# Kernel tuning notes

Hardware: AMD Instinct MI355X
Metric: run time of the kernel (lower is better)

## Reference

```python
import jax, jax.numpy as jnp
import numpy as np

HEADS = 8
NEG = -1e9
EPS = 1e-9


def setup_inputs() -> dict:
    key = jax.random.key(0)
    ks = jax.random.split(key, 24)
    N, D, E = 2048, 512, 64
    s = 0.02
    inp = {
        "xyz": jax.random.normal(ks[0], (N, 3), jnp.float32),
        "str_feat": jax.random.normal(ks[1], (N, D), jnp.float32),
        "esm_feat": jax.random.normal(ks[2], (N, E), jnp.float32),
        "y_hat": jax.random.uniform(ks[3], (N, 1), jnp.float32),
        "distance_mask": jax.random.randint(ks[4], (N, N), 0, 2, jnp.int32),
        "t": jnp.ones((1,), jnp.float32),
        "band_width": jnp.ones((1,), jnp.float32),
        "max_iter": 5,
        # main projections (torch Linear layout: y = x @ W.T + b)
        "Wq": jax.random.normal(ks[5], (D, D), jnp.float32) * s,
        "bq": jnp.zeros((D,), jnp.float32),
        "Wk": jax.random.normal(ks[6], (D, D), jnp.float32) * s,
        "bk": jnp.zeros((D,), jnp.float32),
        "Wv": jax.random.normal(ks[7], (D, D), jnp.float32) * s,
        "bv": jnp.zeros((D,), jnp.float32),
        "Wo": jax.random.normal(ks[8], (D, D), jnp.float32) * s,
        "bo": jnp.zeros((D,), jnp.float32),
        # esm projections (computed in the original forward but unused downstream)
        "Weq": jax.random.normal(ks[9], (E, E), jnp.float32) * s,
        "beq": jnp.zeros((E,), jnp.float32),
        "Wek": jax.random.normal(ks[10], (E, E), jnp.float32) * s,
        "bek": jnp.zeros((E,), jnp.float32),
        "Wev": jax.random.normal(ks[11], (E, E), jnp.float32) * s,
        "bev": jnp.zeros((E,), jnp.float32),
        "Weo": jax.random.normal(ks[12], (E, E), jnp.float32) * s,
        "beo": jnp.zeros((E,), jnp.float32),
    }
    return inp


def reference(xyz, str_feat, esm_feat, y_hat, distance_mask, t, band_width, max_iter,
              Wq, bq, Wk, bk, Wv, bv, Wo, bo,
              Weq, beq, Wek, bek, Wev, bev, Weo, beo):
    N, D = str_feat.shape
    h = HEADS
    dh = D // h

    q = str_feat @ Wq.T + bq
    k = str_feat @ Wk.T + bk
    v = str_feat @ Wv.T + bv
    # esm projections: computed in the original forward but never used (dead code; DCE'd under jit)
    _esm_q = esm_feat @ Weq.T + beq
    _esm_k = esm_feat @ Wek.T + bek
    _esm_v = esm_feat @ Wev.T + bev

    # [h, N, dh]
    qh = q.reshape(N, h, dh).transpose(1, 0, 2)
    kh = k.reshape(N, h, dh).transpose(1, 0, 2)
    vh = v.reshape(N, h, dh).transpose(1, 0, 2)

    scores = jnp.einsum('hnd,hmd->hnm', qh, kh) / jnp.sqrt(jnp.asarray(dh, qh.dtype))
    mask = (distance_mask > 0)[None]              # [1, N, N]
    yw = y_hat[:, 0][None, :]                     # [1, N] per-target weight
    inv_two_bw2 = 1.0 / (2.0 * band_width[0] ** 2)
    temp = t[0]

    def step(carry, _):
        xyz_c, _x = carry
        # squared pairwise distances via the expanded form (avoids [N,N,3])
        sq = jnp.sum(xyz_c * xyz_c, axis=-1)
        d2 = sq[:, None] + sq[None, :] - 2.0 * (xyz_c @ xyz_c.T)
        kern = jnp.exp(-d2 * inv_two_bw2)          # [N, N] band-width kernel
        logits = scores / temp + jnp.log(kern * yw + EPS)[None]
        logits = jnp.where(mask, logits, NEG)
        attn = jax.nn.softmax(logits, axis=-1)     # [h, N, N]
        xyz_new = jnp.einsum('nm,md->nd', attn.mean(0), xyz_c)  # mean-shift step
        x_new = jnp.einsum('hnm,hmd->hnd', attn, vh)            # [h, N, dh]
        return (xyz_new, x_new), None

    (xyz_out, xh), _ = jax.lax.scan(step, (xyz, jnp.zeros_like(vh)), None, length=max_iter)
    x = xh.transpose(1, 0, 2).reshape(N, D)
    out = x @ Wo.T + bo
    return xyz_out, out
```

## Files before the change

kernel.cpp:

```cpp
#include <hip/hip_runtime.h>


typedef __attribute__((ext_vector_type(8))) short bf16x8;
typedef __attribute__((ext_vector_type(4))) float f32x4;

__device__ __forceinline__ unsigned short f2bf(float f) {
    unsigned int u = __float_as_uint(f);
    u += 0x7fff + ((u >> 16) & 1);
    return (unsigned short)(u >> 16);
}
__device__ __forceinline__ float bf2f(unsigned short u) {
    return __uint_as_float((unsigned int)u << 16);
}

union EU { bf16x8 v; unsigned short u[8]; };

__global__ __launch_bounds__(256)
void conv_all(const float* __restrict__ strf,
              const float* __restrict__ Wq, const float* __restrict__ Wk,
              const float* __restrict__ Wv, const float* __restrict__ Wo,
              const int* __restrict__ dmask,
              unsigned short* __restrict__ sA, unsigned short* __restrict__ sW,
              unsigned char* __restrict__ mby)
{
    const long base = (long)(blockIdx.x * 256 + threadIdx.x) * 8;
    if (base >= 2097152) {
        const long rel = base - 2097152;
        int4 a = *reinterpret_cast<const int4*>(dmask + rel);
        int4 b = *reinterpret_cast<const int4*>(dmask + rel + 4);
        unsigned long long p = 0;
        p |= (a.x > 0) ? 0x01ULL : 0;  p |= (a.y > 0) ? 0x0100ULL : 0;
        p |= (a.z > 0) ? 0x010000ULL : 0;  p |= (a.w > 0) ? 0x01000000ULL : 0;
        p |= (b.x > 0) ? 0x0100000000ULL : 0;  p |= (b.y > 0) ? 0x010000000000ULL : 0;
        p |= (b.z > 0) ? 0x01000000000000ULL : 0;  p |= (b.w > 0) ? 0x0100000000000000ULL : 0;
        *reinterpret_cast<unsigned long long*>(mby + rel) = p;
        return;
    }
    const float* src;
    unsigned short* dst;
    if (base < 1048576) {
        src = strf + base; dst = sA + base;
    } else {
        const long rel = base - 1048576;
        const int seg = (int)(rel >> 18);
        const long off = rel & 262143;
        const float* Ws[4] = {Wq, Wk, Wv, Wo};
        src = Ws[seg] + off;
        dst = sW + (long)seg * 262144 + off;
    }
    float4 a = *reinterpret_cast<const float4*>(src);
    float4 b = *reinterpret_cast<const float4*>(src + 4);
    EU o;
    o.u[0] = f2bf(a.x); o.u[1] = f2bf(a.y); o.u[2] = f2bf(a.z); o.u[3] = f2bf(a.w);
    o.u[4] = f2bf(b.x); o.u[5] = f2bf(b.y); o.u[6] = f2bf(b.z); o.u[7] = f2bf(b.w);
    *reinterpret_cast<bf16x8*>(dst) = o.v;
}

__global__ __launch_bounds__(256)
void qkv_mfma(const unsigned short* __restrict__ sA,
              const unsigned short* __restrict__ sW,
              const float* __restrict__ bq, const float* __restrict__ bk,
              const float* __restrict__ bv,
              unsigned short* __restrict__ qh, unsigned short* __restrict__ kh,
              unsigned short* __restrict__ vT)
{
    const int z  = blockIdx.z;
    const int bx = blockIdx.x;
    const int by = blockIdx.y;
    const int tid = threadIdx.x;
    const int wv = tid >> 6;
    const int lane = tid & 63;
    const int row  = lane & 15;
    const int koct = (lane >> 4) * 8;
    const int n0 = bx * 64;

    const unsigned short* Ap = sA + (long)(n0 + wv * 16 + row) * 512;
    const unsigned short* Bp = sW + (long)z * 262144 + (long)(by * 64 + row) * 512;

    f32x4 acc[4] = {};
#pragma unroll
    for (int k0 = 0; k0 < 512; k0 += 32) {
        bf16x8 a = *reinterpret_cast<const bf16x8*>(Ap + k0 + koct);
#pragma unroll
        for (int t = 0; t < 4; t++) {
            bf16x8 b = *reinterpret_cast<const bf16x8*>(Bp + (long)(t * 16) * 512 + k0 + koct);
            acc[t] = __builtin_amdgcn_mfma_f32_16x16x32_bf16(a, b, acc[t], 0, 0, 0);
        }
    }

    if (z == 2) {
        const int rbase = n0 + wv * 16 + (lane >> 4) * 4;
#pragma unroll
        for (int t = 0; t < 4; t++) {
            const int d = by * 64 + t * 16 + (lane & 15);
            const float bb = bv[d];
            ushort4 o;
            o.x = f2bf(acc[t][0] + bb); o.y = f2bf(acc[t][1] + bb);
            o.z = f2bf(acc[t][2] + bb); o.w = f2bf(acc[t][3] + bb);
            *reinterpret_cast<ushort4*>(vT + (long)d * 2048 + rbase) = o;
        }
        return;
    }

    __shared__ float ls[64][68];
    const int lrb = wv * 16 + (lane >> 4) * 4;
    const int lcb = lane & 15;
#pragma unroll
    for (int t = 0; t < 4; t++)
#pragma unroll
        for (int r = 0; r < 4; r++)
            ls[lrb + r][t * 16 + lcb] = acc[t][r];
    __syncthreads();

    const float* bias = (z == 0) ? bq : bk;
    unsigned short* dst = (z == 0) ? qh : kh;
    const int r2 = tid >> 2;
    const int c2 = (tid & 3) * 16;
    float sv[16];
#pragma unroll
    for (int j = 0; j < 4; j++) {
        float4 s = *reinterpret_cast<const float4*>(&ls[r2][c2 + j * 4]);
        float4 bb = *reinterpret_cast<const float4*>(bias + by * 64 + c2 + j * 4);
        sv[j*4+0] = s.x + bb.x; sv[j*4+1] = s.y + bb.y;
        sv[j*4+2] = s.z + bb.z; sv[j*4+3] = s.w + bb.w;
    }
    EU o0, o1;
#pragma unroll
    for (int j = 0; j < 8; j++) { o0.u[j] = f2bf(sv[j]); o1.u[j] = f2bf(sv[8 + j]); }
    unsigned short* dp = dst + (long)(n0 + r2) * 512 + by * 64 + c2;
    *reinterpret_cast<bf16x8*>(dp)     = o0.v;
    *reinterpret_cast<bf16x8*>(dp + 8) = o1.v;
}

__global__ __launch_bounds__(256)
void scores_rows(const unsigned short* __restrict__ qh,
                 const unsigned short* __restrict__ kh,
                 const unsigned char* __restrict__ mby,
                 const float* __restrict__ tptr,
                 unsigned short* __restrict__ Ebf)
{
    const int h  = blockIdx.y;
    const int n0 = blockIdx.x * 16;
    const int tid = threadIdx.x;
    const int wv = tid >> 6;
    const int lane = tid & 63;
    const float scale = 1.0f / (8.0f * tptr[0]);

    __shared__ unsigned short lsb[4][16][260];

    const int arow = lane & 15;
    const int koct = (lane >> 4) * 8;
    const unsigned short* Aq = qh + (long)(n0 + arow) * 512 + h * 64;
    const bf16x8 aq0 = *reinterpret_cast<const bf16x8*>(Aq + koct);
    const bf16x8 aq1 = *reinterpret_cast<const bf16x8*>(Aq + 32 + koct);

    const int lr = (lane >> 4) * 4;
    const int lc = lane & 15;
    const int rlo = lane >> 5;
    const int cch = lane & 31;

#pragma unroll
    for (int half = 0; half < 2; half++) {
        const int mbase = wv * 512 + half * 256;
#pragma unroll
        for (int mt = 0; mt < 16; mt++) {
            const unsigned short* Bk = kh + (long)(mbase + mt * 16 + arow) * 512 + h * 64;
            bf16x8 b0 = *reinterpret_cast<const bf16x8*>(Bk + koct);
            bf16x8 b1 = *reinterpret_cast<const bf16x8*>(Bk + 32 + koct);
            f32x4 c = {};
            c = __builtin_amdgcn_mfma_f32_16x16x32_bf16(aq0, b0, c, 0, 0, 0);
            c = __builtin_amdgcn_mfma_f32_16x16x32_bf16(aq1, b1, c, 0, 0, 0);
#pragma unroll
            for (int r = 0; r < 4; r++)
                lsb[wv][lr + r][mt * 16 + lc] = f2bf(__expf(c[r] * scale));
        }
#pragma unroll
        for (int rp = 0; rp < 8; rp++) {
            const int row = rp * 2 + rlo;
            const int gn = n0 + row;
            const int m = mbase + cch * 8;
            EU e;
            e.v = *reinterpret_cast<const bf16x8*>(&lsb[wv][row][cch * 8]);
            unsigned long long mk =
                *reinterpret_cast<const unsigned long long*>(mby + (long)gn * 2048 + m);
            EU o;
#pragma unroll
            for (int j = 0; j < 8; j++)
                o.u[j] = ((mk >> (8 * j)) & 0xff) ? e.u[j] : (unsigned short)0;
            *reinterpret_cast<bf16x8*>(Ebf + ((long)h * 2048 + gn) * 2048 + m) = o.v;
        }
    }
}

__global__ __launch_bounds__(256)
void ms_iter(const unsigned short* __restrict__ Ebf,
             const float* __restrict__ xyz_src,
             float* __restrict__ xyz_dst,
             const float* __restrict__ y_hat,
             const float* __restrict__ bwp,
             unsigned short* __restrict__ gbf,
             float* __restrict__ invzb,
             int wlast)
{
    const int n = blockIdx.x;
    const int tid = threadIdx.x;
    const int lane = tid & 63;
    const int wave = tid >> 6;
    const int m0 = tid * 8;

    __shared__ float red[64];

    EU E[8];
#pragma unroll
    for (int h = 0; h < 8; h++)
        E[h].v = *reinterpret_cast<const bf16x8*>(Ebf + (long)h * 4194304 + (long)n * 2048 + m0);

    const float bw = bwp[0];
    const float c2k = 1.0f / (2.0f * bw * bw);

    const float xn = xyz_src[n * 3 + 0];
    const float yn = xyz_src[n * 3 + 1];
    const float zn = xyz_src[n * 3 + 2];
    const float sqn = xn * xn + yn * yn + zn * zn;

    float mx[8], my[8], mz[8];
    {
        const float4* xp = reinterpret_cast<const float4*>(xyz_src + (long)m0 * 3);
        float4 a = xp[0], b = xp[1], c = xp[2], d = xp[3], e = xp[4], f = xp[5];
        mx[0]=a.x; my[0]=a.y; mz[0]=a.z;  mx[1]=a.w; my[1]=b.x; mz[1]=b.y;
        mx[2]=b.z; my[2]=b.w; mz[2]=c.x;  mx[3]=c.y; my[3]=c.z; mz[3]=c.w;
        mx[4]=d.x; my[4]=d.y; mz[4]=d.z;  mx[5]=d.w; my[5]=e.x; mz[5]=e.y;
        mx[6]=e.z; my[6]=e.w; mz[6]=f.x;  mx[7]=f.y; my[7]=f.z; mz[7]=f.w;
    }
    float4 yh0 = *reinterpret_cast<const float4*>(y_hat + m0);
    float4 yh1 = *reinterpret_cast<const float4*>(y_hat + m0 + 4);
    float yh[8] = {yh0.x, yh0.y, yh0.z, yh0.w, yh1.x, yh1.y, yh1.z, yh1.w};

    float g[8];
#pragma unroll
    for (int j = 0; j < 8; j++) {
        const float d2 = sqn + (mx[j]*mx[j] + my[j]*my[j] + mz[j]*mz[j])
                       - 2.0f * (xn*mx[j] + yn*my[j] + zn*mz[j]);
        g[j] = __expf(-d2 * c2k) * yh[j] + 1e-9f;
    }

    float z[8];
#pragma unroll
    for (int h = 0; h < 8; h++) {
        float zz = 0.f;
#pragma unroll
        for (int j = 0; j < 8; j++) zz += bf2f(E[h].u[j]) * g[j];
        z[h] = zz;
    }

#pragma unroll
    for (int h = 0; h < 8; h++) {
        float v = z[h];
#pragma unroll
        for (int off = 32; off > 0; off >>= 1) v += __shfl_down(v, off, 64);
        if (lane == 0) red[wave * 8 + h] = v;
    }
    __syncthreads();
    if (tid < 8) {
        const float s = red[tid] + red[8 + tid] + red[16 + tid] + red[24 + tid];
        const float iz = 1.0f / s;
        red[32 + tid] = iz;
        if (wlast) invzb[tid * 2048 + n] = iz;
    }
    __syncthreads();
    float invz[8];
#pragma unroll
    for (int h = 0; h < 8; h++) invz[h] = red[32 + h];
    __syncthreads();

    float ax = 0.f, ay = 0.f, az = 0.f;
#pragma unroll
    for (int j = 0; j < 8; j++) {
        float w = 0.f;
#pragma unroll
        for (int h = 0; h < 8; h++) w += bf2f(E[h].u[j]) * invz[h];
        w *= 0.125f * g[j];
        ax += w * mx[j]; ay += w * my[j]; az += w * mz[j];
    }
    if (wlast) {
        EU og;
#pragma unroll
        for (int j = 0; j < 8; j++) og.u[j] = f2bf(g[j]);
        *reinterpret_cast<bf16x8*>(gbf + (long)n * 2048 + m0) = og.v;
    }

    float v3[3] = {ax, ay, az};
#pragma unroll
    for (int c = 0; c < 3; c++) {
        float v = v3[c];
#pragma unroll
        for (int off = 32; off > 0; off >>= 1) v += __shfl_down(v, off, 64);
        if (lane == 0) red[c * 4 + wave] = v;
    }
    __syncthreads();
    if (tid < 3) {
        xyz_dst[n * 3 + tid] = red[tid * 4 + 0] + red[tid * 4 + 1] +
                               red[tid * 4 + 2] + red[tid * 4 + 3];
    }
}

__global__ __launch_bounds__(256)
void av_mfma(const unsigned short* __restrict__ Ebf,
             const unsigned short* __restrict__ gbf,
             const unsigned short* __restrict__ vT,
             float* __restrict__ P)
{
    const int h  = blockIdx.z;
    const int s  = blockIdx.y;
    const int bx = blockIdx.x;
    const int wv = threadIdx.x >> 6;
    const int lane = threadIdx.x & 63;
    const int n0 = bx * 64 + wv * 16;
    const int kc = s * 512;

    const int mrow = lane & 15;
    const int koct = (lane >> 4) * 8;

    const unsigned short* Ab = Ebf + ((long)h * 2048 + n0 + mrow) * 2048;
    const unsigned short* Gb = gbf + (long)(n0 + mrow) * 2048;
    const unsigned short* Bb = vT + ((long)h * 64 + mrow) * 2048;

    f32x4 acc[4] = {};
    for (int k0 = kc; k0 < kc + 512; k0 += 32) {
        EU e, gg, a;
        e.v  = *reinterpret_cast<const bf16x8*>(Ab + k0 + koct);
        gg.v = *reinterpret_cast<const bf16x8*>(Gb + k0 + koct);
#pragma unroll
        for (int j = 0; j < 8; j++)
            a.u[j] = f2bf(bf2f(e.u[j]) * bf2f(gg.u[j]));
#pragma unroll
        for (int t = 0; t < 4; t++) {
            bf16x8 b = *reinterpret_cast<const bf16x8*>(Bb + (long)(t * 16) * 2048 + k0 + koct);
            acc[t] = __builtin_amdgcn_mfma_f32_16x16x32_bf16(a.v, b, acc[t], 0, 0, 0);
        }
    }

    float* Pp = P + (long)s * 1048576;
    const int rbase = n0 + (lane >> 4) * 4;
    const int dcol = lane & 15;
#pragma unroll
    for (int t = 0; t < 4; t++)
#pragma unroll
        for (int r = 0; r < 4; r++)
            Pp[(long)(rbase + r) * 512 + h * 64 + t * 16 + dcol] = acc[t][r];
}

__global__ __launch_bounds__(256)
void av_red(const float* __restrict__ P, const float* __restrict__ invzb,
            unsigned short* __restrict__ xc)
{
    const long idx = (long)(blockIdx.x * 256 + threadIdx.x) * 8;
    const int n = (int)(idx >> 9);
    const int d0 = (int)(idx & 511);
    const float iz = invzb[(d0 >> 6) * 2048 + n];
    float s[8] = {};
#pragma unroll
    for (int p = 0; p < 4; p++) {
        const float* pp = P + (long)p * 1048576 + idx;
        float4 a = *reinterpret_cast<const float4*>(pp);
        float4 b = *reinterpret_cast<const float4*>(pp + 4);
        s[0] += a.x; s[1] += a.y; s[2] += a.z; s[3] += a.w;
        s[4] += b.x; s[5] += b.y; s[6] += b.z; s[7] += b.w;
    }
    EU o;
#pragma unroll
    for (int j = 0; j < 8; j++) o.u[j] = f2bf(s[j] * iz);
    *reinterpret_cast<bf16x8*>(xc + idx) = o.v;
}

__global__ __launch_bounds__(256)
void out_mfma(const unsigned short* __restrict__ xc,
              const unsigned short* __restrict__ sW,
              const float* __restrict__ bo,
              float* __restrict__ out)
{
    const int bx = blockIdx.x;
    const int by = blockIdx.y;
    const int wv = threadIdx.x >> 6;
    const int lane = threadIdx.x & 63;
    const int row  = lane & 15;
    const int koct = (lane >> 4) * 8;
    const int n0 = bx * 64;

    const unsigned short* Ap = xc + (long)(n0 + wv * 16 + row) * 512;
    const unsigned short* Bp = sW + 3L * 262144 + (long)(by * 64 + row) * 512;

    f32x4 acc[4] = {};
#pragma unroll
    for (int k0 = 0; k0 < 512; k0 += 32) {
        bf16x8 a = *reinterpret_cast<const bf16x8*>(Ap + k0 + koct);
#pragma unroll
        for (int t = 0; t < 4; t++) {
            bf16x8 b = *reinterpret_cast<const bf16x8*>(Bp + (long)(t * 16) * 512 + k0 + koct);
            acc[t] = __builtin_amdgcn_mfma_f32_16x16x32_bf16(a, b, acc[t], 0, 0, 0);
        }
    }

    const int rbase = n0 + wv * 16 + (lane >> 4) * 4;
    const int dcol = lane & 15;
#pragma unroll
    for (int t = 0; t < 4; t++) {
        const int col = by * 64 + t * 16 + dcol;
        const float bb = bo[col];
#pragma unroll
        for (int r = 0; r < 4; r++)
            out[(long)(rbase + r) * 512 + col] = acc[t][r] + bb;
    }
}

extern "C" void kernel_launch(void* const* d_in, const int* in_sizes, int n_in,
                              void* d_out, int out_size, void* d_ws, size_t ws_size,
                              hipStream_t stream)
{
    (void)in_sizes; (void)n_in; (void)out_size; (void)ws_size;

    const float* xyz   = (const float*)d_in[0];
    const float* strf  = (const float*)d_in[1];
    const float* yhat  = (const float*)d_in[3];
    const int*   dmask = (const int*)d_in[4];
    const float* tptr  = (const float*)d_in[5];
    const float* bwptr = (const float*)d_in[6];
    const float* Wq = (const float*)d_in[8];
    const float* bq = (const float*)d_in[9];
    const float* Wk = (const float*)d_in[10];
    const float* bk = (const float*)d_in[11];
    const float* Wv = (const float*)d_in[12];
    const float* bv = (const float*)d_in[13];
    const float* Wo = (const float*)d_in[14];
    const float* bo = (const float*)d_in[15];
    float* outp = (float*)d_out;

    char* wsb = (char*)d_ws;
    float* Ppart         = (float*)(wsb);
    unsigned short* xc   = (unsigned short*)(wsb + (16L << 20));
    unsigned short* sA   = (unsigned short*)(wsb + (18L << 20));
    unsigned short* sW   = (unsigned short*)(wsb + (20L << 20));
    unsigned short* qh   = (unsigned short*)(wsb + (22L << 20));
    unsigned short* kh   = (unsigned short*)(wsb + (24L << 20));
    unsigned short* vT   = (unsigned short*)(wsb + (26L << 20));
    float* xyzA          = (float*)(wsb + (28L << 20));
    float* xyzB          = xyzA + 8192;
    unsigned char* mby   = (unsigned char*)(wsb + (30L << 20));
    unsigned short* Ebf  = (unsigned short*)(wsb + (34L << 20));
    unsigned short* gbf  = (unsigned short*)(wsb + (98L << 20));
    float* invzb         = (float*)(wsb + (106L << 20));

    dim3 blk(256, 1, 1);

    conv_all<<<dim3(3072), blk, 0, stream>>>(strf, Wq, Wk, Wv, Wo, dmask, sA, sW, mby);
    qkv_mfma<<<dim3(32, 8, 3), blk, 0, stream>>>(sA, sW, bq, bk, bv, qh, kh, vT);

    scores_rows<<<dim3(128, 8), blk, 0, stream>>>(qh, kh, mby, tptr, Ebf);

    const float* src = xyz;
    float* dsts[5] = {xyzA, xyzB, xyzA, xyzB, outp};
    for (int it = 0; it < 5; it++) {
        ms_iter<<<dim3(2048), blk, 0, stream>>>(Ebf, src, dsts[it], yhat, bwptr,
                                                gbf, invzb, it == 4 ? 1 : 0);
        src = dsts[it];
    }

    av_mfma<<<dim3(32, 4, 8), blk, 0, stream>>>(Ebf, gbf, vT, Ppart);
    av_red<<<dim3(512), blk, 0, stream>>>(Ppart, invzb, xc);
    out_mfma<<<dim3(32, 8), blk, 0, stream>>>(xc, sW, bo, outp + 6144);
}
```

Measured before the change: 325.3 us.

## Pack four rows per ms_iter block, double split-K in av_mfma with prefetch

```diff
diff --git a/kernel.cpp b/kernel.cpp
--- a/kernel.cpp
+++ b/kernel.cpp
@@ -192,7 +192,7 @@
     }
 }
 
-__global__ __launch_bounds__(256)
+__global__ __launch_bounds__(1024)
 void ms_iter(const unsigned short* __restrict__ Ebf,
              const float* __restrict__ xyz_src,
              float* __restrict__ xyz_dst,
@@ -202,46 +202,47 @@
              float* __restrict__ invzb,
              int wlast)
 {
-    const int n = blockIdx.x;
     const int tid = threadIdx.x;
+    const int rg  = tid >> 8;
+    const int t   = tid & 255;
+    const int n   = blockIdx.x * 4 + rg;
     const int lane = tid & 63;
-    const int wave = tid >> 6;
-    const int m0 = tid * 8;
-
-    __shared__ float red[64];
+    const int wv4 = (t >> 6) & 3;
+    const int m0 = t * 8;
+
+    __shared__ float red[4][52];
 
     EU E[8];
+    const unsigned short* Ep = Ebf + (long)n * 2048 + m0;
 #pragma unroll
     for (int h = 0; h < 8; h++)
-        E[h].v = *reinterpret_cast<const bf16x8*>(Ebf + (long)h * 4194304 + (long)n * 2048 + m0);
+        E[h].v = *reinterpret_cast<const bf16x8*>(Ep + (long)h * 4194304);
 
     const float bw = bwp[0];
     const float c2k = 1.0f / (2.0f * bw * bw);
-
     const float xn = xyz_src[n * 3 + 0];
     const float yn = xyz_src[n * 3 + 1];
     const float zn = xyz_src[n * 3 + 2];
     const float sqn = xn * xn + yn * yn + zn * zn;
 
-    float mx[8], my[8], mz[8];
+    float g[8];
     {
         const float4* xp = reinterpret_cast<const float4*>(xyz_src + (long)m0 * 3);
         float4 a = xp[0], b = xp[1], c = xp[2], d = xp[3], e = xp[4], f = xp[5];
+        float mx[8], my[8], mz[8];
         mx[0]=a.x; my[0]=a.y; mz[0]=a.z;  mx[1]=a.w; my[1]=b.x; mz[1]=b.y;
         mx[2]=b.z; my[2]=b.w; mz[2]=c.x;  mx[3]=c.y; my[3]=c.z; mz[3]=c.w;
         mx[4]=d.x; my[4]=d.y; mz[4]=d.z;  mx[5]=d.w; my[5]=e.x; mz[5]=e.y;
         mx[6]=e.z; my[6]=e.w; mz[6]=f.x;  mx[7]=f.y; my[7]=f.z; mz[7]=f.w;
-    }
-    float4 yh0 = *reinterpret_cast<const float4*>(y_hat + m0);
-    float4 yh1 = *reinterpret_cast<const float4*>(y_hat + m0 + 4);
-    float yh[8] = {yh0.x, yh0.y, yh0.z, yh0.w, yh1.x, yh1.y, yh1.z, yh1.w};
-
-    float g[8];
-#pragma unroll
-    for (int j = 0; j < 8; j++) {
-        const float d2 = sqn + (mx[j]*mx[j] + my[j]*my[j] + mz[j]*mz[j])
-                       - 2.0f * (xn*mx[j] + yn*my[j] + zn*mz[j]);
-        g[j] = __expf(-d2 * c2k) * yh[j] + 1e-9f;
+        float4 yh0 = *reinterpret_cast<const float4*>(y_hat + m0);
+        float4 yh1 = *reinterpret_cast<const float4*>(y_hat + m0 + 4);
+        float yh[8] = {yh0.x, yh0.y, yh0.z, yh0.w, yh1.x, yh1.y, yh1.z, yh1.w};
+#pragma unroll
+        for (int j = 0; j < 8; j++) {
+            const float d2 = sqn + (mx[j]*mx[j] + my[j]*my[j] + mz[j]*mz[j])
+                           - 2.0f * (xn*mx[j] + yn*my[j] + zn*mz[j]);
+            g[j] = __expf(-d2 * c2k) * yh[j] + 1e-9f;
+        }
     }
 
     float z[8];
@@ -258,29 +259,37 @@
         float v = z[h];
 #pragma unroll
         for (int off = 32; off > 0; off >>= 1) v += __shfl_down(v, off, 64);
-        if (lane == 0) red[wave * 8 + h] = v;
+        if (lane == 0) red[rg][wv4 * 8 + h] = v;
     }
     __syncthreads();
-    if (tid < 8) {
-        const float s = red[tid] + red[8 + tid] + red[16 + tid] + red[24 + tid];
+    if (t < 8) {
+        const float s = red[rg][t] + red[rg][8 + t] + red[rg][16 + t] + red[rg][24 + t];
         const float iz = 1.0f / s;
-        red[32 + tid] = iz;
-        if (wlast) invzb[tid * 2048 + n] = iz;
+        red[rg][32 + t] = iz;
+        if (wlast) invzb[t * 2048 + n] = iz;
     }
     __syncthreads();
     float invz[8];
 #pragma unroll
-    for (int h = 0; h < 8; h++) invz[h] = red[32 + h];
-    __syncthreads();
+    for (int h = 0; h < 8; h++) invz[h] = red[rg][32 + h];
 
     float ax = 0.f, ay = 0.f, az = 0.f;
-#pragma unroll
-    for (int j = 0; j < 8; j++) {
-        float w = 0.f;
-#pragma unroll
-        for (int h = 0; h < 8; h++) w += bf2f(E[h].u[j]) * invz[h];
-        w *= 0.125f * g[j];
-        ax += w * mx[j]; ay += w * my[j]; az += w * mz[j];
+    {
+        const float4* xp = reinterpret_cast<const float4*>(xyz_src + (long)m0 * 3);
+        float4 a = xp[0], b = xp[1], c = xp[2], d = xp[3], e = xp[4], f = xp[5];
+        float mx[8], my[8], mz[8];
+        mx[0]=a.x; my[0]=a.y; mz[0]=a.z;  mx[1]=a.w; my[1]=b.x; mz[1]=b.y;
+        mx[2]=b.z; my[2]=b.w; mz[2]=c.x;  mx[3]=c.y; my[3]=c.z; mz[3]=c.w;
+        mx[4]=d.x; my[4]=d.y; mz[4]=d.z;  mx[5]=d.w; my[5]=e.x; mz[5]=e.y;
+        mx[6]=e.z; my[6]=e.w; mz[6]=f.x;  mx[7]=f.y; my[7]=f.z; mz[7]=f.w;
+#pragma unroll
+        for (int j = 0; j < 8; j++) {
+            float w = 0.f;
+#pragma unroll
+            for (int h = 0; h < 8; h++) w += bf2f(E[h].u[j]) * invz[h];
+            w *= 0.125f * g[j];
+            ax += w * mx[j]; ay += w * my[j]; az += w * mz[j];
+        }
     }
     if (wlast) {
         EU og;
@@ -295,12 +304,12 @@
         float v = v3[c];
 #pragma unroll
         for (int off = 32; off > 0; off >>= 1) v += __shfl_down(v, off, 64);
-        if (lane == 0) red[c * 4 + wave] = v;
+        if (lane == 0) red[rg][40 + c * 4 + wv4] = v;
     }
     __syncthreads();
-    if (tid < 3) {
-        xyz_dst[n * 3 + tid] = red[tid * 4 + 0] + red[tid * 4 + 1] +
-                               red[tid * 4 + 2] + red[tid * 4 + 3];
+    if (t < 3) {
+        xyz_dst[n * 3 + t] = red[rg][40 + t * 4 + 0] + red[rg][40 + t * 4 + 1] +
+                             red[rg][40 + t * 4 + 2] + red[rg][40 + t * 4 + 3];
     }
 }
 
@@ -316,28 +325,36 @@
     const int wv = threadIdx.x >> 6;
     const int lane = threadIdx.x & 63;
     const int n0 = bx * 64 + wv * 16;
-    const int kc = s * 512;
+    const int kc = s * 256;
 
     const int mrow = lane & 15;
     const int koct = (lane >> 4) * 8;
 
-    const unsigned short* Ab = Ebf + ((long)h * 2048 + n0 + mrow) * 2048;
-    const unsigned short* Gb = gbf + (long)(n0 + mrow) * 2048;
-    const unsigned short* Bb = vT + ((long)h * 64 + mrow) * 2048;
+    const unsigned short* Ab = Ebf + ((long)h * 2048 + n0 + mrow) * 2048 + kc + koct;
+    const unsigned short* Gb = gbf + (long)(n0 + mrow) * 2048 + kc + koct;
+    const unsigned short* Bb = vT + ((long)h * 64 + mrow) * 2048 + kc + koct;
 
     f32x4 acc[4] = {};
-    for (int k0 = kc; k0 < kc + 512; k0 += 32) {
-        EU e, gg, a;
-        e.v  = *reinterpret_cast<const bf16x8*>(Ab + k0 + koct);
-        gg.v = *reinterpret_cast<const bf16x8*>(Gb + k0 + koct);
+    EU e0, g0;
+    e0.v = *reinterpret_cast<const bf16x8*>(Ab);
+    g0.v = *reinterpret_cast<const bf16x8*>(Gb);
+#pragma unroll
+    for (int ki = 0; ki < 8; ki++) {
+        EU e1, g1;
+        if (ki < 7) {
+            e1.v = *reinterpret_cast<const bf16x8*>(Ab + (ki + 1) * 32);
+            g1.v = *reinterpret_cast<const bf16x8*>(Gb + (ki + 1) * 32);
+        }
+        EU a;
 #pragma unroll
         for (int j = 0; j < 8; j++)
-            a.u[j] = f2bf(bf2f(e.u[j]) * bf2f(gg.u[j]));
+            a.u[j] = f2bf(bf2f(e0.u[j]) * bf2f(g0.u[j]));
 #pragma unroll
         for (int t = 0; t < 4; t++) {
-            bf16x8 b = *reinterpret_cast<const bf16x8*>(Bb + (long)(t * 16) * 2048 + k0 + koct);
+            bf16x8 b = *reinterpret_cast<const bf16x8*>(Bb + (long)(t * 16) * 2048 + ki * 32);
             acc[t] = __builtin_amdgcn_mfma_f32_16x16x32_bf16(a.v, b, acc[t], 0, 0, 0);
         }
+        e0 = e1; g0 = g1;
     }
 
     float* Pp = P + (long)s * 1048576;
@@ -360,7 +377,7 @@
     const float iz = invzb[(d0 >> 6) * 2048 + n];
     float s[8] = {};
 #pragma unroll
-    for (int p = 0; p < 4; p++) {
+    for (int p = 0; p < 8; p++) {
         const float* pp = P + (long)p * 1048576 + idx;
         float4 a = *reinterpret_cast<const float4*>(pp);
         float4 b = *reinterpret_cast<const float4*>(pp + 4);
@@ -437,18 +454,18 @@
 
     char* wsb = (char*)d_ws;
     float* Ppart         = (float*)(wsb);
-    unsigned short* xc   = (unsigned short*)(wsb + (16L << 20));
-    unsigned short* sA   = (unsigned short*)(wsb + (18L << 20));
-    unsigned short* sW   = (unsigned short*)(wsb + (20L << 20));
-    unsigned short* qh   = (unsigned short*)(wsb + (22L << 20));
-    unsigned short* kh   = (unsigned short*)(wsb + (24L << 20));
-    unsigned short* vT   = (unsigned short*)(wsb + (26L << 20));
-    float* xyzA          = (float*)(wsb + (28L << 20));
+    unsigned short* xc   = (unsigned short*)(wsb + (32L << 20));
+    unsigned short* sA   = (unsigned short*)(wsb + (34L << 20));
+    unsigned short* sW   = (unsigned short*)(wsb + (36L << 20));
+    unsigned short* qh   = (unsigned short*)(wsb + (38L << 20));
+    unsigned short* kh   = (unsigned short*)(wsb + (40L << 20));
+    unsigned short* vT   = (unsigned short*)(wsb + (42L << 20));
+    float* xyzA          = (float*)(wsb + (44L << 20));
     float* xyzB          = xyzA + 8192;
-    unsigned char* mby   = (unsigned char*)(wsb + (30L << 20));
-    unsigned short* Ebf  = (unsigned short*)(wsb + (34L << 20));
-    unsigned short* gbf  = (unsigned short*)(wsb + (98L << 20));
-    float* invzb         = (float*)(wsb + (106L << 20));
+    unsigned char* mby   = (unsigned char*)(wsb + (45L << 20));
+    unsigned short* Ebf  = (unsigned short*)(wsb + (49L << 20));
+    unsigned short* gbf  = (unsigned short*)(wsb + (113L << 20));
+    float* invzb         = (float*)(wsb + (121L << 20));
 
     dim3 blk(256, 1, 1);
 
@@ -460,12 +477,12 @@
     const float* src = xyz;
     float* dsts[5] = {xyzA, xyzB, xyzA, xyzB, outp};
     for (int it = 0; it < 5; it++) {
-        ms_iter<<<dim3(2048), blk, 0, stream>>>(Ebf, src, dsts[it], yhat, bwptr,
-                                                gbf, invzb, it == 4 ? 1 : 0);
+        ms_iter<<<dim3(512), dim3(1024), 0, stream>>>(Ebf, src, dsts[it], yhat, bwptr,
+                                                      gbf, invzb, it == 4 ? 1 : 0);
         src = dsts[it];
     }
 
-    av_mfma<<<dim3(32, 4, 8), blk, 0, stream>>>(Ebf, gbf, vT, Ppart);
+    av_mfma<<<dim3(32, 8, 8), blk, 0, stream>>>(Ebf, gbf, vT, Ppart);
     av_red<<<dim3(512), blk, 0, stream>>>(Ppart, invzb, xc);
     out_mfma<<<dim3(32, 8), blk, 0, stream>>>(xc, sW, bo, outp + 6144);
 }
```

Result: slower. 342.3 us (+5.2%).
